# Optimization experiments

Measured on AMD Instinct MI355X. Metric: run time of the kernel, lower is better.

The kernel has to match this reference:

```python
import jax, jax.numpy as jnp
import numpy as np

B, TM1, ENC, DEC, OUT = 256, 32, 128, 128, 1


def setup_inputs() -> dict:
    key = jax.random.key(0)
    ks = jax.random.split(key, 16)
    s = 0.05
    inp = {
        "input_encoded": jax.random.normal(ks[0], (B, TM1, ENC), jnp.float32),
        "y_history": jax.random.normal(ks[1], (B, TM1, OUT), jnp.float32),
        # attn_layer: Linear(2*DEC+ENC -> ENC), Tanh, Linear(ENC -> 1)
        "attn_W1": jax.random.normal(ks[2], (ENC, 2 * DEC + ENC), jnp.float32) * s,
        "attn_b1": jnp.zeros((ENC,), jnp.float32),
        "attn_W2": jax.random.normal(ks[3], (1, ENC), jnp.float32) * s,
        "attn_b2": jnp.zeros((1,), jnp.float32),
        # LSTM(input_size=OUT, hidden_size=DEC), pytorch gate order i,f,g,o
        "W_ih": jax.random.normal(ks[4], (4 * DEC, OUT), jnp.float32) * s,
        "W_hh": jax.random.normal(ks[5], (4 * DEC, DEC), jnp.float32) * s,
        "b_ih": jnp.zeros((4 * DEC,), jnp.float32),
        "b_hh": jnp.zeros((4 * DEC,), jnp.float32),
        # fc: Linear(ENC+OUT -> OUT), weight initialized with normal_() in torch
        "fc_W": jax.random.normal(ks[6], (OUT, ENC + OUT), jnp.float32),
        "fc_b": jnp.zeros((OUT,), jnp.float32),
        # fc_final: Linear(DEC+ENC -> OUT)
        "fcf_W": jax.random.normal(ks[7], (OUT, DEC + ENC), jnp.float32) * s,
        "fcf_b": jnp.zeros((OUT,), jnp.float32),
    }
    return inp


def _forward(input_encoded, y_history, attn_W1, attn_b1, attn_W2, attn_b2,
             W_ih, W_hh, b_ih, b_hh, fc_W, fc_b, fcf_W, fcf_b):
    b, tm1, enc = input_encoded.shape
    dec = W_hh.shape[1]

    h0 = jnp.zeros((b, dec), input_encoded.dtype)
    c0 = jnp.zeros((b, dec), input_encoded.dtype)
    ctx0 = jnp.zeros((b, enc), input_encoded.dtype)

    def step(carry, y_t):  # y_t: [B, OUT]
        h, c, _ = carry
        hc = jnp.concatenate([h, c], axis=-1)  # [B, 2*DEC]
        x = jnp.concatenate(
            [jnp.broadcast_to(hc[:, None, :], (b, tm1, 2 * dec)), input_encoded],
            axis=-1)  # [B, T-1, 2*DEC+ENC]
        hdn = jnp.tanh(jnp.einsum('bte,he->bth', x, attn_W1) + attn_b1)
        logits = jnp.einsum('bth,oh->bto', hdn, attn_W2)[..., 0] + attn_b2[0]  # [B, T-1]
        attn = jax.nn.softmax(logits, axis=1)
        ctx = jnp.einsum('bt,bte->be', attn, input_encoded)  # [B, ENC]
        y_tilde = jnp.concatenate([ctx, y_t], axis=1) @ fc_W.T + fc_b  # [B, OUT]
        gates = y_tilde @ W_ih.T + b_ih + h @ W_hh.T + b_hh  # [B, 4*DEC]
        i, f, g, o = jnp.split(gates, 4, axis=-1)
        c_new = jax.nn.sigmoid(f) * c + jax.nn.sigmoid(i) * jnp.tanh(g)
        h_new = jax.nn.sigmoid(o) * jnp.tanh(c_new)
        return (h_new, c_new, ctx), None

    (h, c, ctx), _ = jax.lax.scan(step, (h0, c0, ctx0),
                                  jnp.swapaxes(y_history, 0, 1))
    out = jnp.concatenate([h, ctx], axis=1) @ fcf_W.T + fcf_b + y_history[:, -1]
    return out  # [B, OUT]


def reference(input_encoded, y_history, attn_W1, attn_b1, attn_W2, attn_b2,
              W_ih, W_hh, b_ih, b_hh, fc_W, fc_b, fcf_W, fcf_b):
    return _forward(input_encoded, y_history, attn_W1, attn_b1, attn_W2, attn_b2,
                    W_ih, W_hh, b_ih, b_hh, fc_W, fc_b, fcf_W, fcf_b)
```

## Files before the change

### kernel.cpp

```cpp
#include <hip/hip_runtime.h>


#define TT 32

typedef _Float16 h2_t __attribute__((ext_vector_type(2)));
typedef _Float16 h4_t __attribute__((ext_vector_type(4)));
typedef _Float16 h8_t __attribute__((ext_vector_type(8)));

#if __has_builtin(__builtin_amdgcn_fdot2)
#define FDOT2(a, b, c) __builtin_amdgcn_fdot2((a), (b), (c), false)
#else
static __device__ __forceinline__ float FDOT2(h2_t a, h2_t b, float c) {
    return c + (float)a[0] * (float)b[0] + (float)a[1] * (float)b[1];
}
#endif

__device__ __forceinline__ float dot_h8(h8_t w, h8_t v, float acc) {
    acc = FDOT2(__builtin_shufflevector(w, w, 0, 1), __builtin_shufflevector(v, v, 0, 1), acc);
    acc = FDOT2(__builtin_shufflevector(w, w, 2, 3), __builtin_shufflevector(v, v, 2, 3), acc);
    acc = FDOT2(__builtin_shufflevector(w, w, 4, 5), __builtin_shufflevector(v, v, 4, 5), acc);
    acc = FDOT2(__builtin_shufflevector(w, w, 6, 7), __builtin_shufflevector(v, v, 6, 7), acc);
    return acc;
}
__device__ __forceinline__ h8_t pk8(float4 a, float4 b) {
    h8_t r;
    r[0] = (_Float16)a.x; r[1] = (_Float16)a.y; r[2] = (_Float16)a.z; r[3] = (_Float16)a.w;
    r[4] = (_Float16)b.x; r[5] = (_Float16)b.y; r[6] = (_Float16)b.z; r[7] = (_Float16)b.w;
    return r;
}
__device__ __forceinline__ float fast_tanh(float x) {
    float e = __expf(2.f * x);
    return 1.f - __fdividef(2.f, e + 1.f);
}
__device__ __forceinline__ float fast_sig(float x) {
    return __fdividef(1.f, 1.f + __expf(-x));
}

__global__ __launch_bounds__(512, 2) void decoder_kernel(
    const float* __restrict__ enc_g,
    const float* __restrict__ yh_g,
    const float* __restrict__ W1,
    const float* __restrict__ b1,
    const float* __restrict__ W2,
    const float* __restrict__ b2,
    const float* __restrict__ Wih,
    const float* __restrict__ Whh,
    const float* __restrict__ bih,
    const float* __restrict__ bhh,
    const float* __restrict__ fcW,
    const float* __restrict__ fcB,
    const float* __restrict__ fcfW,
    const float* __restrict__ fcfB,
    float* __restrict__ out)
{
    __shared__ __align__(16) _Float16 s_enc16[TT * 136];
    __shared__ __align__(16) _Float16 s_epre16[TT * 128];
    __shared__ __align__(16) _Float16 s_hc[2 * 272];
    __shared__ __align__(16) _Float16 s_A16[128];
    __shared__ __align__(16) _Float16 s_w216[128];
    __shared__ __align__(16) float s_gdot3[384];
    __shared__ float s_logit[TT];
    __shared__ float s_q[TT];
    __shared__ float s_att[TT];
    __shared__ float s_yh[TT];
    __shared__ float s_ctx[128];

    const int tid = threadIdx.x;
    const int b = blockIdx.x;
    const int lane = tid & 63;
    const int g1 = tid >> 2, s4 = tid & 3;

    {
        const float4* encp = (const float4*)(enc_g + (size_t)b * TT * 128);
#pragma unroll
        for (int r = 0; r < 2; r++) {
            int gi = tid * 2 + r;
            float4 v = encp[gi];
            int t = gi >> 5, e4 = gi & 31;
            h4_t hv;
            hv[0] = (_Float16)v.x; hv[1] = (_Float16)v.y;
            hv[2] = (_Float16)v.z; hv[3] = (_Float16)v.w;
            *(h4_t*)(s_enc16 + t * 136 + e4 * 4) = hv;
        }
    }
    if (tid < 272) ((unsigned int*)s_hc)[tid] = 0u;
    if (tid < 128) s_w216[tid] = (_Float16)W2[tid];
    if (tid < TT) s_yh[tid] = yh_g[b * TT + tid];

    h8_t whhreg[16];
    {
        const float4* wp = (const float4*)(Whh + (size_t)tid * 128);
#pragma unroll
        for (int k = 0; k < 16; k++) whhreg[k] = pk8(wp[2 * k], wp[2 * k + 1]);
    }
    const float bias_r = bih[tid] + bhh[tid];

    h8_t w1areg[8];
    {
        const float4* p = (const float4*)(W1 + g1 * 384 + s4 * 64);
#pragma unroll
        for (int k = 0; k < 8; k++) w1areg[k] = pk8(p[2 * k], p[2 * k + 1]);
    }

    float wih0 = 0.f, wih1 = 0.f, wih2 = 0.f, wih3 = 0.f;
    if (tid < 128) {
        wih0 = Wih[tid];
        wih1 = Wih[128 + tid];
        wih2 = Wih[256 + tid];
        wih3 = Wih[384 + tid];
    }
    const float b2v = b2[0];
    const float fcw128 = fcW[128];
    const float fcbv = fcB[0];
    const float fcfbv = fcfB[0];
    __syncthreads();

    {
        const float4* wp = (const float4*)(W1 + g1 * 384 + 256 + s4 * 32);
        h8_t wa = pk8(wp[0], wp[1]), wb = pk8(wp[2], wp[3]);
        h8_t wc = pk8(wp[4], wp[5]), wd = pk8(wp[6], wp[7]);
        const float b1v = b1[g1];
        for (int t = 0; t < TT; t++) {
            const h8_t* ep8 = (const h8_t*)(s_enc16 + t * 136);
            float pa = dot_h8(wa, ep8[s4 * 4 + 0], 0.f);
            float pb = dot_h8(wb, ep8[s4 * 4 + 1], 0.f);
            pa = dot_h8(wc, ep8[s4 * 4 + 2], pa);
            pb = dot_h8(wd, ep8[s4 * 4 + 3], pb);
            float pp = pa + pb;
            pp += __shfl_xor(pp, 1);
            pp += __shfl_xor(pp, 2);
            if (s4 == 0) s_epre16[t * 128 + g1] = (_Float16)(pp + b1v);
        }
    }
    if (tid < 128) {
        const int tq = tid >> 2, sq = tid & 3;
        const float4* fp = (const float4*)(fcW + sq * 32);
        h8_t fa = pk8(fp[0], fp[1]), fb = pk8(fp[2], fp[3]);
        h8_t fc2 = pk8(fp[4], fp[5]), fd = pk8(fp[6], fp[7]);
        const h8_t* ep8 = (const h8_t*)(s_enc16 + tq * 136);
        float pa = dot_h8(fa, ep8[sq * 4 + 0], 0.f);
        float pb = dot_h8(fb, ep8[sq * 4 + 1], 0.f);
        pa = dot_h8(fc2, ep8[sq * 4 + 2], pa);
        pb = dot_h8(fd, ep8[sq * 4 + 3], pb);
        float pq = pa + pb;
        pq += __shfl_xor(pq, 1);
        pq += __shfl_xor(pq, 2);
        if (sq == 0) s_q[tq] = pq;
    }
    float c_reg = 0.f;
    __syncthreads();

    for (int t = 0; t < TT; t++) {
        float gdot, aa;
        {
            const h8_t* hp0 = (const h8_t*)s_hc;
            const h8_t* hpA = (const h8_t*)(s_hc + (s4 & 1) * 272);
            float a0 = 0.f, a1 = 0.f;
            float g0 = 0.f, g1v = 0.f, g2 = 0.f, g3 = 0.f;
#pragma unroll
            for (int k = 0; k < 4; k++) {
                a0 = dot_h8(w1areg[2 * k], hpA[s4 * 8 + 2 * k], a0);
                a1 = dot_h8(w1areg[2 * k + 1], hpA[s4 * 8 + 2 * k + 1], a1);
                g0 = dot_h8(whhreg[4 * k + 0], hp0[4 * k + 0], g0);
                g1v = dot_h8(whhreg[4 * k + 1], hp0[4 * k + 1], g1v);
                g2 = dot_h8(whhreg[4 * k + 2], hp0[4 * k + 2], g2);
                g3 = dot_h8(whhreg[4 * k + 3], hp0[4 * k + 3], g3);
            }
            gdot = (g0 + g1v) + (g2 + g3) + bias_r;
            aa = a0 + a1;
            aa += __shfl_xor(aa, 1);
            aa += __shfl_xor(aa, 2);
        }
        if (s4 == 0) s_A16[g1] = (_Float16)aa;
        if (tid >= 128) s_gdot3[tid - 128] = gdot;
        __syncthreads();

        {
            const int tt_ = tid >> 4, sub = tid & 15;
            h8_t ev = ((const h8_t*)(s_epre16 + tt_ * 128))[sub];
            h8_t av = ((const h8_t*)s_A16)[sub];
            h8_t wv = ((const h8_t*)s_w216)[sub];
            float lp = 0.f;
#pragma unroll
            for (int i = 0; i < 8; i++)
                lp += (float)wv[i] * fast_tanh((float)av[i] + (float)ev[i]);
            lp += __shfl_xor(lp, 1);
            lp += __shfl_xor(lp, 2);
            lp += __shfl_xor(lp, 4);
            lp += __shfl_xor(lp, 8);
            if (sub == 0) s_logit[tt_] = lp + b2v;
        }
        __syncthreads();

        if (tid < 128) {
            float el = __expf(s_logit[lane & 31]);
            float ql = s_q[lane & 31];
            float ss = el, ys = el * ql;
#pragma unroll
            for (int m = 1; m <= 16; m <<= 1) {
                ss += __shfl_xor(ss, m);
                ys += __shfl_xor(ys, m);
            }
            float inv = __fdividef(1.f, ss);
            if (t == TT - 1 && tid < TT) s_att[tid] = el * inv;
            float yt = ys * inv + fcw128 * s_yh[t] + fcbv;
            float gi_ = gdot + wih0 * yt;
            float gf_ = s_gdot3[tid] + wih1 * yt;
            float gg_ = s_gdot3[128 + tid] + wih2 * yt;
            float go_ = s_gdot3[256 + tid] + wih3 * yt;
            float cn = fast_sig(gf_) * c_reg + fast_sig(gi_) * fast_tanh(gg_);
            float hn = fast_sig(go_) * fast_tanh(cn);
            c_reg = cn;
            _Float16 hh = (_Float16)hn, cc = (_Float16)cn;
            s_hc[tid] = hh;
            s_hc[128 + tid] = cc;
            s_hc[272 + tid] = hh;
            s_hc[400 + tid] = cc;
        }
        __syncthreads();
    }

    if (tid < 128) {
        float acc = 0.f;
#pragma unroll 8
        for (int t2 = 0; t2 < TT; t2++) acc += s_att[t2] * (float)s_enc16[t2 * 136 + tid];
        s_ctx[tid] = acc;
    }
    __syncthreads();
    if (tid < 64) {
        float p = fcfW[lane] * (float)s_hc[lane] +
                  fcfW[64 + lane] * (float)s_hc[64 + lane] +
                  fcfW[128 + lane] * s_ctx[lane] +
                  fcfW[192 + lane] * s_ctx[64 + lane];
#pragma unroll
        for (int m = 1; m < 64; m <<= 1) p += __shfl_xor(p, m);
        if (lane == 0) out[b] = p + fcfbv + s_yh[TT - 1];
    }
}

extern "C" void kernel_launch(void* const* d_in, const int* in_sizes, int n_in,
                              void* d_out, int out_size, void* d_ws, size_t ws_size,
                              hipStream_t stream) {
    decoder_kernel<<<256, 512, 0, stream>>>(
        (const float*)d_in[0], (const float*)d_in[1], (const float*)d_in[2],
        (const float*)d_in[3], (const float*)d_in[4], (const float*)d_in[5],
        (const float*)d_in[6], (const float*)d_in[7], (const float*)d_in[8],
        (const float*)d_in[9], (const float*)d_in[10], (const float*)d_in[11],
        (const float*)d_in[12], (const float*)d_in[13], (float*)d_out);
}
```

Baseline: 166.0 us.

## Split W_hh matvec across 4 lanes per hidden unit with shuffle reduction

```diff
diff --git a/kernel.cpp b/kernel.cpp
--- a/kernel.cpp
+++ b/kernel.cpp
@@ -55,10 +55,9 @@
 {
     __shared__ __align__(16) _Float16 s_enc16[TT * 136];
     __shared__ __align__(16) _Float16 s_epre16[TT * 128];
-    __shared__ __align__(16) _Float16 s_hc[2 * 272];
+    __shared__ __align__(16) _Float16 s_hcx[4 * 264];
     __shared__ __align__(16) _Float16 s_A16[128];
     __shared__ __align__(16) _Float16 s_w216[128];
-    __shared__ __align__(16) float s_gdot3[384];
     __shared__ float s_logit[TT];
     __shared__ float s_q[TT];
     __shared__ float s_att[TT];
@@ -68,7 +67,7 @@
     const int tid = threadIdx.x;
     const int b = blockIdx.x;
     const int lane = tid & 63;
-    const int g1 = tid >> 2, s4 = tid & 3;
+    const int g = tid >> 2, s4 = tid & 3;
 
     {
         const float4* encp = (const float4*)(enc_g + (size_t)b * TT * 128);
@@ -83,31 +82,25 @@
             *(h4_t*)(s_enc16 + t * 136 + e4 * 4) = hv;
         }
     }
-    if (tid < 272) ((unsigned int*)s_hc)[tid] = 0u;
+    for (int i = tid; i < 528; i += 512) ((unsigned int*)s_hcx)[i] = 0u;
     if (tid < 128) s_w216[tid] = (_Float16)W2[tid];
     if (tid < TT) s_yh[tid] = yh_g[b * TT + tid];
 
-    h8_t whhreg[16];
-    {
-        const float4* wp = (const float4*)(Whh + (size_t)tid * 128);
-#pragma unroll
-        for (int k = 0; k < 16; k++) whhreg[k] = pk8(wp[2 * k], wp[2 * k + 1]);
-    }
-    const float bias_r = bih[tid] + bhh[tid];
-
     h8_t w1areg[8];
     {
-        const float4* p = (const float4*)(W1 + g1 * 384 + s4 * 64);
+        const float4* p = (const float4*)(W1 + g * 384 + s4 * 64);
 #pragma unroll
         for (int k = 0; k < 8; k++) w1areg[k] = pk8(p[2 * k], p[2 * k + 1]);
     }
-
-    float wih0 = 0.f, wih1 = 0.f, wih2 = 0.f, wih3 = 0.f;
-    if (tid < 128) {
-        wih0 = Wih[tid];
-        wih1 = Wih[128 + tid];
-        wih2 = Wih[256 + tid];
-        wih3 = Wih[384 + tid];
+    h8_t whhreg[4][4];
+    float biasr[4], wihr[4];
+#pragma unroll
+    for (int j = 0; j < 4; j++) {
+        const float4* p = (const float4*)(Whh + (size_t)(j * 128 + g) * 128 + s4 * 32);
+#pragma unroll
+        for (int k = 0; k < 4; k++) whhreg[j][k] = pk8(p[2 * k], p[2 * k + 1]);
+        biasr[j] = bih[j * 128 + g] + bhh[j * 128 + g];
+        wihr[j] = Wih[j * 128 + g];
     }
     const float b2v = b2[0];
     const float fcw128 = fcW[128];
@@ -116,10 +109,10 @@
     __syncthreads();
 
     {
-        const float4* wp = (const float4*)(W1 + g1 * 384 + 256 + s4 * 32);
+        const float4* wp = (const float4*)(W1 + g * 384 + 256 + s4 * 32);
         h8_t wa = pk8(wp[0], wp[1]), wb = pk8(wp[2], wp[3]);
         h8_t wc = pk8(wp[4], wp[5]), wd = pk8(wp[6], wp[7]);
-        const float b1v = b1[g1];
+        const float b1v = b1[g];
         for (int t = 0; t < TT; t++) {
             const h8_t* ep8 = (const h8_t*)(s_enc16 + t * 136);
             float pa = dot_h8(wa, ep8[s4 * 4 + 0], 0.f);
@@ -129,7 +122,7 @@
             float pp = pa + pb;
             pp += __shfl_xor(pp, 1);
             pp += __shfl_xor(pp, 2);
-            if (s4 == 0) s_epre16[t * 128 + g1] = (_Float16)(pp + b1v);
+            if (s4 == 0) s_epre16[t * 128 + g] = (_Float16)(pp + b1v);
         }
     }
     if (tid < 128) {
@@ -151,28 +144,41 @@
     __syncthreads();
 
     for (int t = 0; t < TT; t++) {
-        float gdot, aa;
+        float gd0, gd1, gd2, gd3;
         {
-            const h8_t* hp0 = (const h8_t*)s_hc;
-            const h8_t* hpA = (const h8_t*)(s_hc + (s4 & 1) * 272);
+            const h8_t* hx = ((const h8_t*)s_hcx) + s4 * 33;
             float a0 = 0.f, a1 = 0.f;
-            float g0 = 0.f, g1v = 0.f, g2 = 0.f, g3 = 0.f;
+            float gp0 = 0.f, gp1 = 0.f, gp2 = 0.f, gp3 = 0.f;
 #pragma unroll
             for (int k = 0; k < 4; k++) {
-                a0 = dot_h8(w1areg[2 * k], hpA[s4 * 8 + 2 * k], a0);
-                a1 = dot_h8(w1areg[2 * k + 1], hpA[s4 * 8 + 2 * k + 1], a1);
-                g0 = dot_h8(whhreg[4 * k + 0], hp0[4 * k + 0], g0);
-                g1v = dot_h8(whhreg[4 * k + 1], hp0[4 * k + 1], g1v);
-                g2 = dot_h8(whhreg[4 * k + 2], hp0[4 * k + 2], g2);
-                g3 = dot_h8(whhreg[4 * k + 3], hp0[4 * k + 3], g3);
-            }
-            gdot = (g0 + g1v) + (g2 + g3) + bias_r;
-            aa = a0 + a1;
+                a0 = dot_h8(w1areg[2 * k], hx[s4 * 8 + 2 * k], a0);
+                a1 = dot_h8(w1areg[2 * k + 1], hx[s4 * 8 + 2 * k + 1], a1);
+            }
+#pragma unroll
+            for (int k = 0; k < 4; k++) {
+                h8_t hv = hx[s4 * 4 + k];
+                gp0 = dot_h8(whhreg[0][k], hv, gp0);
+                gp1 = dot_h8(whhreg[1][k], hv, gp1);
+                gp2 = dot_h8(whhreg[2][k], hv, gp2);
+                gp3 = dot_h8(whhreg[3][k], hv, gp3);
+            }
+            float aa = a0 + a1;
             aa += __shfl_xor(aa, 1);
             aa += __shfl_xor(aa, 2);
-        }
-        if (s4 == 0) s_A16[g1] = (_Float16)aa;
-        if (tid >= 128) s_gdot3[tid - 128] = gdot;
+            gp0 += __shfl_xor(gp0, 1);
+            gp0 += __shfl_xor(gp0, 2);
+            gp1 += __shfl_xor(gp1, 1);
+            gp1 += __shfl_xor(gp1, 2);
+            gp2 += __shfl_xor(gp2, 1);
+            gp2 += __shfl_xor(gp2, 2);
+            gp3 += __shfl_xor(gp3, 1);
+            gp3 += __shfl_xor(gp3, 2);
+            if (s4 == 0) s_A16[g] = (_Float16)aa;
+            gd0 = gp0 + biasr[0];
+            gd1 = gp1 + biasr[1];
+            gd2 = gp2 + biasr[2];
+            gd3 = gp3 + biasr[3];
+        }
         __syncthreads();
 
         {
@@ -192,7 +198,7 @@
         }
         __syncthreads();
 
-        if (tid < 128) {
+        {
             float el = __expf(s_logit[lane & 31]);
             float ql = s_q[lane & 31];
             float ss = el, ys = el * ql;
@@ -204,18 +210,21 @@
             float inv = __fdividef(1.f, ss);
             if (t == TT - 1 && tid < TT) s_att[tid] = el * inv;
             float yt = ys * inv + fcw128 * s_yh[t] + fcbv;
-            float gi_ = gdot + wih0 * yt;
-            float gf_ = s_gdot3[tid] + wih1 * yt;
-            float gg_ = s_gdot3[128 + tid] + wih2 * yt;
-            float go_ = s_gdot3[256 + tid] + wih3 * yt;
-            float cn = fast_sig(gf_) * c_reg + fast_sig(gi_) * fast_tanh(gg_);
-            float hn = fast_sig(go_) * fast_tanh(cn);
-            c_reg = cn;
-            _Float16 hh = (_Float16)hn, cc = (_Float16)cn;
-            s_hc[tid] = hh;
-            s_hc[128 + tid] = cc;
-            s_hc[272 + tid] = hh;
-            s_hc[400 + tid] = cc;
+            if (s4 == 0) {
+                float gi_ = gd0 + wihr[0] * yt;
+                float gf_ = gd1 + wihr[1] * yt;
+                float gg_ = gd2 + wihr[2] * yt;
+                float go_ = gd3 + wihr[3] * yt;
+                float cn = fast_sig(gf_) * c_reg + fast_sig(gi_) * fast_tanh(gg_);
+                float hn = fast_sig(go_) * fast_tanh(cn);
+                c_reg = cn;
+                _Float16 hh = (_Float16)hn, cc = (_Float16)cn;
+#pragma unroll
+                for (int j = 0; j < 4; j++) {
+                    s_hcx[j * 264 + g] = hh;
+                    s_hcx[j * 264 + 128 + g] = cc;
+                }
+            }
         }
         __syncthreads();
     }
@@ -228,8 +237,8 @@
     }
     __syncthreads();
     if (tid < 64) {
-        float p = fcfW[lane] * (float)s_hc[lane] +
-                  fcfW[64 + lane] * (float)s_hc[64 + lane] +
+        float p = fcfW[lane] * (float)s_hcx[lane] +
+                  fcfW[64 + lane] * (float)s_hcx[64 + lane] +
                   fcfW[128 + lane] * s_ctx[lane] +
                   fcfW[192 + lane] * s_ctx[64 + lane];
 #pragma unroll
```

Result: slower. 171.5 us (+3.3%).

## Use MFMA for recurrent and attention matvecs with 1024-thread blocks

Applied to the files above, without the earlier changes.

```diff
diff --git a/kernel.cpp b/kernel.cpp
--- a/kernel.cpp
+++ b/kernel.cpp
@@ -5,7 +5,8 @@
 
 typedef _Float16 h2_t __attribute__((ext_vector_type(2)));
 typedef _Float16 h4_t __attribute__((ext_vector_type(4)));
-typedef _Float16 h8_t __attribute__((ext_vector_type(8)));
+typedef _Float16 f16x8 __attribute__((ext_vector_type(8)));
+typedef float f32x4 __attribute__((ext_vector_type(4)));
 
 #if __has_builtin(__builtin_amdgcn_fdot2)
 #define FDOT2(a, b, c) __builtin_amdgcn_fdot2((a), (b), (c), false)
@@ -15,15 +16,15 @@
 }
 #endif
 
-__device__ __forceinline__ float dot_h8(h8_t w, h8_t v, float acc) {
+__device__ __forceinline__ float dot_h8(f16x8 w, f16x8 v, float acc) {
     acc = FDOT2(__builtin_shufflevector(w, w, 0, 1), __builtin_shufflevector(v, v, 0, 1), acc);
     acc = FDOT2(__builtin_shufflevector(w, w, 2, 3), __builtin_shufflevector(v, v, 2, 3), acc);
     acc = FDOT2(__builtin_shufflevector(w, w, 4, 5), __builtin_shufflevector(v, v, 4, 5), acc);
     acc = FDOT2(__builtin_shufflevector(w, w, 6, 7), __builtin_shufflevector(v, v, 6, 7), acc);
     return acc;
 }
-__device__ __forceinline__ h8_t pk8(float4 a, float4 b) {
-    h8_t r;
+__device__ __forceinline__ f16x8 pk8(float4 a, float4 b) {
+    f16x8 r;
     r[0] = (_Float16)a.x; r[1] = (_Float16)a.y; r[2] = (_Float16)a.z; r[3] = (_Float16)a.w;
     r[4] = (_Float16)b.x; r[5] = (_Float16)b.y; r[6] = (_Float16)b.z; r[7] = (_Float16)b.w;
     return r;
@@ -36,7 +37,9 @@
     return __fdividef(1.f, 1.f + __expf(-x));
 }
 
-__global__ __launch_bounds__(512, 2) void decoder_kernel(
+#define MFMA(a, b, c) __builtin_amdgcn_mfma_f32_16x16x32_f16((a), (b), (c), 0, 0, 0)
+
+__global__ __launch_bounds__(1024, 4) void decoder_kernel(
     const float* __restrict__ enc_g,
     const float* __restrict__ yh_g,
     const float* __restrict__ W1,
@@ -54,61 +57,36 @@
     float* __restrict__ out)
 {
     __shared__ __align__(16) _Float16 s_enc16[TT * 136];
-    __shared__ __align__(16) _Float16 s_epre16[TT * 128];
-    __shared__ __align__(16) _Float16 s_hc[2 * 272];
+    __shared__ __align__(16) _Float16 s_epre16[TT * 132];
+    __shared__ __align__(16) _Float16 s_hc16[256];
     __shared__ __align__(16) _Float16 s_A16[128];
     __shared__ __align__(16) _Float16 s_w216[128];
-    __shared__ __align__(16) float s_gdot3[384];
-    __shared__ float s_logit[TT];
-    __shared__ float s_q[TT];
-    __shared__ float s_att[TT];
+    __shared__ __align__(16) float s_gdot[512];
+    __shared__ __align__(16) float s_elog[TT];
+    __shared__ __align__(16) float s_eq[TT];
+    __shared__ __align__(16) float s_qf[TT];
     __shared__ float s_yh[TT];
     __shared__ float s_ctx[128];
 
     const int tid = threadIdx.x;
     const int b = blockIdx.x;
     const int lane = tid & 63;
-    const int g1 = tid >> 2, s4 = tid & 3;
+    const int wv = tid >> 6;
+    const int lrow = lane & 15;
+    const int lk = lane >> 4;
 
     {
         const float4* encp = (const float4*)(enc_g + (size_t)b * TT * 128);
-#pragma unroll
-        for (int r = 0; r < 2; r++) {
-            int gi = tid * 2 + r;
-            float4 v = encp[gi];
-            int t = gi >> 5, e4 = gi & 31;
-            h4_t hv;
-            hv[0] = (_Float16)v.x; hv[1] = (_Float16)v.y;
-            hv[2] = (_Float16)v.z; hv[3] = (_Float16)v.w;
-            *(h4_t*)(s_enc16 + t * 136 + e4 * 4) = hv;
-        }
-    }
-    if (tid < 272) ((unsigned int*)s_hc)[tid] = 0u;
+        float4 v = encp[tid];
+        int t = tid >> 5, e4 = tid & 31;
+        h4_t hv;
+        hv[0] = (_Float16)v.x; hv[1] = (_Float16)v.y;
+        hv[2] = (_Float16)v.z; hv[3] = (_Float16)v.w;
+        *(h4_t*)(s_enc16 + t * 136 + e4 * 4) = hv;
+    }
+    if (tid < 256) s_hc16[tid] = (_Float16)0.f;
     if (tid < 128) s_w216[tid] = (_Float16)W2[tid];
     if (tid < TT) s_yh[tid] = yh_g[b * TT + tid];
-
-    h8_t whhreg[16];
-    {
-        const float4* wp = (const float4*)(Whh + (size_t)tid * 128);
-#pragma unroll
-        for (int k = 0; k < 16; k++) whhreg[k] = pk8(wp[2 * k], wp[2 * k + 1]);
-    }
-    const float bias_r = bih[tid] + bhh[tid];
-
-    h8_t w1areg[8];
-    {
-        const float4* p = (const float4*)(W1 + g1 * 384 + s4 * 64);
-#pragma unroll
-        for (int k = 0; k < 8; k++) w1areg[k] = pk8(p[2 * k], p[2 * k + 1]);
-    }
-
-    float wih0 = 0.f, wih1 = 0.f, wih2 = 0.f, wih3 = 0.f;
-    if (tid < 128) {
-        wih0 = Wih[tid];
-        wih1 = Wih[128 + tid];
-        wih2 = Wih[256 + tid];
-        wih3 = Wih[384 + tid];
-    }
     const float b2v = b2[0];
     const float fcw128 = fcW[128];
     const float fcbv = fcB[0];
@@ -116,120 +94,170 @@
     __syncthreads();
 
     {
-        const float4* wp = (const float4*)(W1 + g1 * 384 + 256 + s4 * 32);
-        h8_t wa = pk8(wp[0], wp[1]), wb = pk8(wp[2], wp[3]);
-        h8_t wc = pk8(wp[4], wp[5]), wd = pk8(wp[6], wp[7]);
-        const float b1v = b1[g1];
-        for (int t = 0; t < TT; t++) {
-            const h8_t* ep8 = (const h8_t*)(s_enc16 + t * 136);
-            float pa = dot_h8(wa, ep8[s4 * 4 + 0], 0.f);
-            float pb = dot_h8(wb, ep8[s4 * 4 + 1], 0.f);
-            pa = dot_h8(wc, ep8[s4 * 4 + 2], pa);
-            pb = dot_h8(wd, ep8[s4 * 4 + 3], pb);
-            float pp = pa + pb;
-            pp += __shfl_xor(pp, 1);
-            pp += __shfl_xor(pp, 2);
-            if (s4 == 0) s_epre16[t * 128 + g1] = (_Float16)(pp + b1v);
-        }
-    }
+        const int rt = wv >> 1, ct = wv & 1;
+        f32x4 cE = {0.f, 0.f, 0.f, 0.f};
+#pragma unroll
+        for (int kt = 0; kt < 4; kt++) {
+            const float* ap = W1 + (16 * rt + lrow) * 384 + 256 + 32 * kt + 8 * lk;
+            f16x8 af = pk8(*(const float4*)ap, *(const float4*)(ap + 4));
+            f16x8 bf = *(const f16x8*)(s_enc16 + (16 * ct + lrow) * 136 + 32 * kt + 8 * lk);
+            cE = MFMA(af, bf, cE);
+        }
+        float4 b1v = *(const float4*)(b1 + 16 * rt + 4 * lk);
+        h4_t o;
+        o[0] = (_Float16)(cE[0] + b1v.x);
+        o[1] = (_Float16)(cE[1] + b1v.y);
+        o[2] = (_Float16)(cE[2] + b1v.z);
+        o[3] = (_Float16)(cE[3] + b1v.w);
+        const int tcol = 16 * ct + lrow;
+        *(h4_t*)(s_epre16 + tcol * 132 + 16 * rt + 4 * lk) = o;
+    }
+
     if (tid < 128) {
         const int tq = tid >> 2, sq = tid & 3;
         const float4* fp = (const float4*)(fcW + sq * 32);
-        h8_t fa = pk8(fp[0], fp[1]), fb = pk8(fp[2], fp[3]);
-        h8_t fc2 = pk8(fp[4], fp[5]), fd = pk8(fp[6], fp[7]);
-        const h8_t* ep8 = (const h8_t*)(s_enc16 + tq * 136);
-        float pa = dot_h8(fa, ep8[sq * 4 + 0], 0.f);
-        float pb = dot_h8(fb, ep8[sq * 4 + 1], 0.f);
-        pa = dot_h8(fc2, ep8[sq * 4 + 2], pa);
-        pb = dot_h8(fd, ep8[sq * 4 + 3], pb);
+        f16x8 fa_ = pk8(fp[0], fp[1]), fb_ = pk8(fp[2], fp[3]);
+        f16x8 fc_ = pk8(fp[4], fp[5]), fd_ = pk8(fp[6], fp[7]);
+        const f16x8* ep8 = (const f16x8*)(s_enc16 + tq * 136);
+        float pa = dot_h8(fa_, ep8[sq * 4 + 0], 0.f);
+        float pb = dot_h8(fb_, ep8[sq * 4 + 1], 0.f);
+        pa = dot_h8(fc_, ep8[sq * 4 + 2], pa);
+        pb = dot_h8(fd_, ep8[sq * 4 + 3], pb);
         float pq = pa + pb;
         pq += __shfl_xor(pq, 1);
         pq += __shfl_xor(pq, 2);
-        if (sq == 0) s_q[tq] = pq;
+        if (sq == 0) s_qf[tq] = pq;
+    }
+
+    f16x8 wf[16];
+    if (wv < 8) {
+#pragma unroll
+        for (int rt = 0; rt < 4; rt++)
+#pragma unroll
+            for (int kt = 0; kt < 4; kt++) {
+                const float* p = Whh + (size_t)(64 * wv + 16 * rt + lrow) * 128 + 32 * kt + 8 * lk;
+                wf[rt * 4 + kt] = pk8(*(const float4*)p, *(const float4*)(p + 4));
+            }
+    } else {
+        const int wa = wv - 8;
+#pragma unroll
+        for (int kt = 0; kt < 8; kt++) {
+            const float* p = W1 + (16 * wa + lrow) * 384 + 32 * kt + 8 * lk;
+            wf[kt] = pk8(*(const float4*)p, *(const float4*)(p + 4));
+        }
+    }
+    float biasr0 = 0.f, biasr1 = 0.f, biasr2 = 0.f, biasr3 = 0.f;
+    float wihr0 = 0.f, wihr1 = 0.f, wihr2 = 0.f, wihr3 = 0.f;
+    if (tid < 128) {
+        biasr0 = bih[tid] + bhh[tid];
+        biasr1 = bih[128 + tid] + bhh[128 + tid];
+        biasr2 = bih[256 + tid] + bhh[256 + tid];
+        biasr3 = bih[384 + tid] + bhh[384 + tid];
+        wihr0 = Wih[tid]; wihr1 = Wih[128 + tid];
+        wihr2 = Wih[256 + tid]; wihr3 = Wih[384 + tid];
     }
     float c_reg = 0.f;
     __syncthreads();
 
     for (int t = 0; t < TT; t++) {
-        float gdot, aa;
+        if (wv < 8) {
+            f16x8 hb0 = *(const f16x8*)(s_hc16 + 0 + 8 * lk);
+            f16x8 hb1 = *(const f16x8*)(s_hc16 + 32 + 8 * lk);
+            f16x8 hb2 = *(const f16x8*)(s_hc16 + 64 + 8 * lk);
+            f16x8 hb3 = *(const f16x8*)(s_hc16 + 96 + 8 * lk);
+            f32x4 c0 = {0.f, 0.f, 0.f, 0.f}, c1 = c0, c2 = c0, c3 = c0;
+            c0 = MFMA(wf[0], hb0, c0);  c1 = MFMA(wf[4], hb0, c1);
+            c2 = MFMA(wf[8], hb0, c2);  c3 = MFMA(wf[12], hb0, c3);
+            c0 = MFMA(wf[1], hb1, c0);  c1 = MFMA(wf[5], hb1, c1);
+            c2 = MFMA(wf[9], hb1, c2);  c3 = MFMA(wf[13], hb1, c3);
+            c0 = MFMA(wf[2], hb2, c0);  c1 = MFMA(wf[6], hb2, c1);
+            c2 = MFMA(wf[10], hb2, c2); c3 = MFMA(wf[14], hb2, c3);
+            c0 = MFMA(wf[3], hb3, c0);  c1 = MFMA(wf[7], hb3, c1);
+            c2 = MFMA(wf[11], hb3, c2); c3 = MFMA(wf[15], hb3, c3);
+            if (lrow == 0) {
+                *(f32x4*)(s_gdot + 64 * wv + 0 + 4 * lk) = c0;
+                *(f32x4*)(s_gdot + 64 * wv + 16 + 4 * lk) = c1;
+                *(f32x4*)(s_gdot + 64 * wv + 32 + 4 * lk) = c2;
+                *(f32x4*)(s_gdot + 64 * wv + 48 + 4 * lk) = c3;
+            }
+        } else {
+            const int wa = wv - 8;
+            f32x4 ca = {0.f, 0.f, 0.f, 0.f};
+#pragma unroll
+            for (int kt = 0; kt < 8; kt++) {
+                f16x8 hb = *(const f16x8*)(s_hc16 + kt * 32 + 8 * lk);
+                ca = MFMA(wf[kt], hb, ca);
+            }
+            if (lrow == 0) {
+                h4_t o;
+                o[0] = (_Float16)ca[0]; o[1] = (_Float16)ca[1];
+                o[2] = (_Float16)ca[2]; o[3] = (_Float16)ca[3];
+                *(h4_t*)(s_A16 + 16 * wa + 4 * lk) = o;
+            }
+        }
+        __syncthreads();
+
         {
-            const h8_t* hp0 = (const h8_t*)s_hc;
-            const h8_t* hpA = (const h8_t*)(s_hc + (s4 & 1) * 272);
-            float a0 = 0.f, a1 = 0.f;
-            float g0 = 0.f, g1v = 0.f, g2 = 0.f, g3 = 0.f;
-#pragma unroll
-            for (int k = 0; k < 4; k++) {
-                a0 = dot_h8(w1areg[2 * k], hpA[s4 * 8 + 2 * k], a0);
-                a1 = dot_h8(w1areg[2 * k + 1], hpA[s4 * 8 + 2 * k + 1], a1);
-                g0 = dot_h8(whhreg[4 * k + 0], hp0[4 * k + 0], g0);
-                g1v = dot_h8(whhreg[4 * k + 1], hp0[4 * k + 1], g1v);
-                g2 = dot_h8(whhreg[4 * k + 2], hp0[4 * k + 2], g2);
-                g3 = dot_h8(whhreg[4 * k + 3], hp0[4 * k + 3], g3);
-            }
-            gdot = (g0 + g1v) + (g2 + g3) + bias_r;
-            aa = a0 + a1;
-            aa += __shfl_xor(aa, 1);
-            aa += __shfl_xor(aa, 2);
-        }
-        if (s4 == 0) s_A16[g1] = (_Float16)aa;
-        if (tid >= 128) s_gdot3[tid - 128] = gdot;
-        __syncthreads();
-
-        {
-            const int tt_ = tid >> 4, sub = tid & 15;
-            h8_t ev = ((const h8_t*)(s_epre16 + tt_ * 128))[sub];
-            h8_t av = ((const h8_t*)s_A16)[sub];
-            h8_t wv = ((const h8_t*)s_w216)[sub];
-            float lp = 0.f;
-#pragma unroll
-            for (int i = 0; i < 8; i++)
-                lp += (float)wv[i] * fast_tanh((float)av[i] + (float)ev[i]);
+            const int tt_ = tid >> 5, sub = tid & 31;
+            h4_t ev = *(const h4_t*)(s_epre16 + tt_ * 132 + sub * 4);
+            h4_t av = *(const h4_t*)(s_A16 + sub * 4);
+            h4_t wv2 = *(const h4_t*)(s_w216 + sub * 4);
+            float lp = (float)wv2[0] * fast_tanh((float)av[0] + (float)ev[0]) +
+                       (float)wv2[1] * fast_tanh((float)av[1] + (float)ev[1]) +
+                       (float)wv2[2] * fast_tanh((float)av[2] + (float)ev[2]) +
+                       (float)wv2[3] * fast_tanh((float)av[3] + (float)ev[3]);
             lp += __shfl_xor(lp, 1);
             lp += __shfl_xor(lp, 2);
             lp += __shfl_xor(lp, 4);
             lp += __shfl_xor(lp, 8);
-            if (sub == 0) s_logit[tt_] = lp + b2v;
+            lp += __shfl_xor(lp, 16);
+            if (sub == 0) {
+                float el = __expf(lp + b2v);
+                s_elog[tt_] = el;
+                s_eq[tt_] = el * s_qf[tt_];
+            }
         }
         __syncthreads();
 
         if (tid < 128) {
-            float el = __expf(s_logit[lane & 31]);
-            float ql = s_q[lane & 31];
-            float ss = el, ys = el * ql;
-#pragma unroll
-            for (int m = 1; m <= 16; m <<= 1) {
-                ss += __shfl_xor(ss, m);
-                ys += __shfl_xor(ys, m);
-            }
-            float inv = __fdividef(1.f, ss);
-            if (t == TT - 1 && tid < TT) s_att[tid] = el * inv;
-            float yt = ys * inv + fcw128 * s_yh[t] + fcbv;
-            float gi_ = gdot + wih0 * yt;
-            float gf_ = s_gdot3[tid] + wih1 * yt;
-            float gg_ = s_gdot3[128 + tid] + wih2 * yt;
-            float go_ = s_gdot3[256 + tid] + wih3 * yt;
+            float gdi = s_gdot[tid];
+            float gdf = s_gdot[128 + tid];
+            float gdg = s_gdot[256 + tid];
+            float gdo = s_gdot[384 + tid];
+            const f32x4* ep = (const f32x4*)s_elog;
+            const f32x4* qp = (const f32x4*)s_eq;
+            f32x4 se = (ep[0] + ep[1]) + (ep[2] + ep[3]) + (ep[4] + ep[5]) + (ep[6] + ep[7]);
+            f32x4 sy = (qp[0] + qp[1]) + (qp[2] + qp[3]) + (qp[4] + qp[5]) + (qp[6] + qp[7]);
+            float ss = (se[0] + se[1]) + (se[2] + se[3]);
+            float ys = (sy[0] + sy[1]) + (sy[2] + sy[3]);
+            float yt = __fdividef(ys, ss) + fcw128 * s_yh[t] + fcbv;
+            float gi_ = gdi + biasr0 + wihr0 * yt;
+            float gf_ = gdf + biasr1 + wihr1 * yt;
+            float gg_ = gdg + biasr2 + wihr2 * yt;
+            float go_ = gdo + biasr3 + wihr3 * yt;
             float cn = fast_sig(gf_) * c_reg + fast_sig(gi_) * fast_tanh(gg_);
             float hn = fast_sig(go_) * fast_tanh(cn);
             c_reg = cn;
-            _Float16 hh = (_Float16)hn, cc = (_Float16)cn;
-            s_hc[tid] = hh;
-            s_hc[128 + tid] = cc;
-            s_hc[272 + tid] = hh;
-            s_hc[400 + tid] = cc;
+            s_hc16[tid] = (_Float16)hn;
+            s_hc16[128 + tid] = (_Float16)cn;
         }
         __syncthreads();
     }
 
     if (tid < 128) {
+        const f32x4* ep = (const f32x4*)s_elog;
+        f32x4 se = (ep[0] + ep[1]) + (ep[2] + ep[3]) + (ep[4] + ep[5]) + (ep[6] + ep[7]);
+        float inv = __fdividef(1.f, (se[0] + se[1]) + (se[2] + se[3]));
         float acc = 0.f;
 #pragma unroll 8
-        for (int t2 = 0; t2 < TT; t2++) acc += s_att[t2] * (float)s_enc16[t2 * 136 + tid];
-        s_ctx[tid] = acc;
+        for (int t2 = 0; t2 < TT; t2++)
+            acc += s_elog[t2] * (float)s_enc16[t2 * 136 + tid];
+        s_ctx[tid] = acc * inv;
     }
     __syncthreads();
     if (tid < 64) {
-        float p = fcfW[lane] * (float)s_hc[lane] +
-                  fcfW[64 + lane] * (float)s_hc[64 + lane] +
+        float p = fcfW[lane] * (float)s_hc16[lane] +
+                  fcfW[64 + lane] * (float)s_hc16[64 + lane] +
                   fcfW[128 + lane] * s_ctx[lane] +
                   fcfW[192 + lane] * s_ctx[64 + lane];
 #pragma unroll
@@ -241,7 +269,7 @@
 extern "C" void kernel_launch(void* const* d_in, const int* in_sizes, int n_in,
                               void* d_out, int out_size, void* d_ws, size_t ws_size,
                               hipStream_t stream) {
-    decoder_kernel<<<256, 512, 0, stream>>>(
+    decoder_kernel<<<256, 1024, 0, stream>>>(
         (const float*)d_in[0], (const float*)d_in[1], (const float*)d_in[2],
         (const float*)d_in[3], (const float*)d_in[4], (const float*)d_in[5],
         (const float*)d_in[6], (const float*)d_in[7], (const float*)d_in[8],
```

Result: faster. 159.2 us (-4.1%).
